# Performance work log

Measured on AMD Instinct MI355X. Metric: run time of the kernel, lower is better.

## Reference

```python
import jax, jax.numpy as jnp
import numpy as np

N = 100000          # total nodes
F = 128             # in_features
B = 1000            # number of graphs
NPG = 100           # nodes per graph (contiguous)
DEG = 16            # avg degree
E = B * NPG * DEG   # total edges (intra-graph)
K_RATIO = 0.8
KNUM = max(1, int(K_RATIO * NPG))  # nodes kept per graph = 80


def setup_inputs() -> dict:
    key = jax.random.key(0)
    k1, k2, k3, k4 = jax.random.split(key, 4)
    x = jax.random.normal(k1, (N, F), dtype=jnp.float32)
    # intra-graph random edges: offset each block of NPG*DEG edges by its graph's base node id
    offs = (jnp.arange(E, dtype=jnp.int32) // (NPG * DEG)) * NPG
    src = jax.random.randint(k2, (E,), 0, NPG, dtype=jnp.int32) + offs
    dst = jax.random.randint(k3, (E,), 0, NPG, dtype=jnp.int32) + offs
    edge_index = jnp.stack([src, dst], axis=0)
    batch = (jnp.arange(N, dtype=jnp.int32) // NPG).astype(jnp.int32)
    limit = float(np.sqrt(6.0 / (F + 1)))  # xavier_uniform for (F,1)
    theta_att = jax.random.uniform(k4, (F, 1), dtype=jnp.float32, minval=-limit, maxval=limit)
    return {"x": x, "edge_index": edge_index, "batch": batch, "theta_att": theta_att}


def reference(x, edge_index, batch, theta_att):
    num_nodes = x.shape[0]
    # add self loops with weight 1
    loops = jnp.arange(num_nodes, dtype=edge_index.dtype)
    row = jnp.concatenate([edge_index[0], loops])
    col = jnp.concatenate([edge_index[1], loops])
    w = jnp.ones(row.shape[0], dtype=x.dtype)
    # symmetric degree normalization (degree counted over row, as in torch code)
    deg = jax.ops.segment_sum(w, row, num_segments=num_nodes)
    dis = jnp.where(deg > 0, jax.lax.rsqrt(deg), jnp.zeros((), x.dtype))
    norm = dis[row] * w * dis[col]
    # scatter-add: agg[dst] += x[src] * norm
    agg = jax.ops.segment_sum(x[row] * norm[:, None], col, num_segments=num_nodes)
    z = (agg @ theta_att)[:, 0]                     # (N,)
    # per-graph top-k: graphs are contiguous and equal-sized -> reshape
    zb = z.reshape(B, NPG)
    _, pos = jax.lax.top_k(zb, KNUM)                # (B, KNUM) positions within each graph
    pos = jnp.sort(pos, axis=1)                     # global sort of keep_idx == per-graph sort here
    keep = (pos + jnp.arange(B, dtype=pos.dtype)[:, None] * NPG).reshape(-1)  # (B*KNUM,)
    scale = jax.nn.sigmoid(z[keep])[:, None]
    x_new = x[keep] * scale                         # (B*KNUM, F)
    batch_new = batch[keep]
    # subgraph with relabeled nodes; dropped edges padded with -1 (fixed shape for jit)
    node_mask = jnp.zeros(num_nodes, dtype=bool).at[keep].set(True)
    new_id = jnp.cumsum(node_mask.astype(jnp.int32)) - 1
    emask = node_mask[edge_index[0]] & node_mask[edge_index[1]]
    edge_index_new = jnp.where(emask[None, :], new_id[edge_index], -1)
    return x_new, edge_index_new, batch_new
```

## Files before the change

kernel.cpp:

```cpp
#include <hip/hip_runtime.h>


#define NPG   100
#define EPG   1600
#define KNUM  80
#define FDIM  128
#define NF4   (NPG * FDIM / 4)
#define NE4   (EPG / 4)

__global__ __launch_bounds__(256)
void sagpool_fused3(const float* __restrict__ x,
                    const int*   __restrict__ ei,
                    const float* __restrict__ theta,
                    float* __restrict__ out,
                    int E_total, int out_x_elems)
{
    const int g    = blockIdx.x;
    const int tid  = threadIdx.x;
    const int wave = tid >> 6;
    const int lane = tid & 63;
    const int base = g * NPG;

    __shared__ int4   sh_edge4[NE4];
    __shared__ int    sh_deg[NPG];
    __shared__ double sh_s[NPG];
    __shared__ double sh_dis[NPG];
    __shared__ double sh_a[NPG];
    __shared__ double sh_zp[4][NPG];
    __shared__ double sh_z[NPG];
    __shared__ unsigned long long sh_mask[2];
    __shared__ int    sh_newid[NPG];
    __shared__ int    sh_keepnode[KNUM];
    __shared__ float  sh_scale[KNUM];

    int* sh_edge = (int*)sh_edge4;

    const float4 th = ((const float4*)theta)[lane & 31];

    if (tid < NPG) sh_deg[tid] = 1;
    for (int i = tid; i < 4 * NPG; i += 256) ((double*)sh_zp)[i] = 0.0;
    __syncthreads();

    const int4* src4 = (const int4*)(ei + (size_t)g * EPG);
    const int4* dst4 = (const int4*)(ei + (size_t)E_total + (size_t)g * EPG);
    const bool  hasE1 = tid < (NE4 - 256);
    int4 es0 = src4[tid];
    int4 ed0 = dst4[tid];
    int4 es1, ed1;
    if (hasE1) { es1 = src4[256 + tid]; ed1 = dst4[256 + tid]; }

    const float4* xb4 = (const float4*)(x + (size_t)base * FDIM);
    float4 v[12];
    #pragma unroll
    for (int i = 0; i < 12; ++i) v[i] = xb4[i * 256 + tid];
    const bool has13 = tid < (NF4 - 12 * 256);
    float4 v12;
    if (has13) v12 = xb4[12 * 256 + tid];

    {
        int4 s4 = es0, d4 = ed0;
        s4.x -= base; s4.y -= base; s4.z -= base; s4.w -= base;
        d4.x -= base; d4.y -= base; d4.z -= base; d4.w -= base;
        int4 p; p.x = s4.x | (d4.x << 16); p.y = s4.y | (d4.y << 16);
                p.z = s4.z | (d4.z << 16); p.w = s4.w | (d4.w << 16);
        sh_edge4[tid] = p;
        atomicAdd(&sh_deg[s4.x], 1); atomicAdd(&sh_deg[s4.y], 1);
        atomicAdd(&sh_deg[s4.z], 1); atomicAdd(&sh_deg[s4.w], 1);
    }
    if (hasE1) {
        int4 s4 = es1, d4 = ed1;
        s4.x -= base; s4.y -= base; s4.z -= base; s4.w -= base;
        d4.x -= base; d4.y -= base; d4.z -= base; d4.w -= base;
        int4 p; p.x = s4.x | (d4.x << 16); p.y = s4.y | (d4.y << 16);
                p.z = s4.z | (d4.z << 16); p.w = s4.w | (d4.w << 16);
        sh_edge4[256 + tid] = p;
        atomicAdd(&sh_deg[s4.x], 1); atomicAdd(&sh_deg[s4.y], 1);
        atomicAdd(&sh_deg[s4.z], 1); atomicAdd(&sh_deg[s4.w], 1);
    }

    #pragma unroll
    for (int i = 0; i < 12; ++i) {
        double p = (double)v[i].x * th.x + (double)v[i].y * th.y
                 + (double)v[i].z * th.z + (double)v[i].w * th.w;
        #pragma unroll
        for (int m = 1; m <= 16; m <<= 1) p += __shfl_xor(p, m, 64);
        if ((lane & 31) == 0) sh_s[(i * 256 + tid) >> 5] = p;
    }
    if (tid < 128) {
        double p = (double)v12.x * th.x + (double)v12.y * th.y
                 + (double)v12.z * th.z + (double)v12.w * th.w;
        #pragma unroll
        for (int m = 1; m <= 16; m <<= 1) p += __shfl_xor(p, m, 64);
        if ((lane & 31) == 0) sh_s[(12 * 256 + tid) >> 5] = p;
    }
    __syncthreads();

    if (tid < NPG) {
        double dis = 1.0 / sqrt((double)sh_deg[tid]);
        sh_dis[tid] = dis;
        sh_a[tid]   = sh_s[tid] * dis;
    }
    __syncthreads();

    {
        double* zp = sh_zp[wave];
        for (int j = tid; j < EPG; j += 256) {
            int p = sh_edge[j];
            int s = p & 0xffff;
            int d = p >> 16;
            atomicAdd(&zp[d], sh_a[s] * sh_dis[d]);
        }
    }
    __syncthreads();

    double zi = 0.0;
    if (tid < NPG) {
        zi = sh_a[tid] * sh_dis[tid]
           + sh_zp[0][tid] + sh_zp[1][tid] + sh_zp[2][tid] + sh_zp[3][tid];
        sh_z[tid] = zi;
    }
    __syncthreads();

    bool kept = false;
    if (tid < NPG) {
        int rank = 0;
        for (int j = 0; j < NPG; ++j) {
            double zj = sh_z[j];
            rank += (int)((zj > zi) | ((zj == zi) & (j < tid)));
        }
        kept = rank < KNUM;
        sh_newid[tid] = -1;
    }
    unsigned long long m = __ballot(kept);
    if (lane == 0 && wave < 2) sh_mask[wave] = m;
    __syncthreads();

    if (kept) {
        int before = (wave == 0)
            ? __popcll(sh_mask[0] & ((1ull << lane) - 1ull))
            : __popcll(sh_mask[0]) + __popcll(sh_mask[1] & ((1ull << lane) - 1ull));
        int row = g * KNUM + before;
        sh_newid[tid]       = row;
        sh_keepnode[before] = tid;
        sh_scale[before]    = (float)(1.0 / (1.0 + exp(-zi)));
        out[(size_t)out_x_elems + 2 * (size_t)E_total + row] = (float)g;
    }
    __syncthreads();

    for (int idx = tid; idx < KNUM * FDIM / 4; idx += 256) {
        int   row  = idx >> 5;
        int   c    = idx & 31;
        int   node = sh_keepnode[row];
        float sc   = sh_scale[row];
        float4 xv  = ((const float4*)(x + (size_t)(base + node) * FDIM))[c];
        float4 o;
        o.x = xv.x * sc; o.y = xv.y * sc; o.z = xv.z * sc; o.w = xv.w * sc;
        ((float4*)(out + (size_t)(g * KNUM + row) * FDIM))[c] = o;
    }

    float* e0 = out + out_x_elems;
    float* e1 = e0 + E_total;
    for (int slot = tid; slot < NE4; slot += 256) {
        int4 p = sh_edge4[slot];
        float4 o0, o1;
        {
            int s = p.x & 0xffff, d = p.x >> 16;
            int a = sh_newid[s], b = sh_newid[d];
            bool vv = (a >= 0) && (b >= 0);
            o0.x = vv ? (float)a : -1.0f; o1.x = vv ? (float)b : -1.0f;
        }
        {
            int s = p.y & 0xffff, d = p.y >> 16;
            int a = sh_newid[s], b = sh_newid[d];
            bool vv = (a >= 0) && (b >= 0);
            o0.y = vv ? (float)a : -1.0f; o1.y = vv ? (float)b : -1.0f;
        }
        {
            int s = p.z & 0xffff, d = p.z >> 16;
            int a = sh_newid[s], b = sh_newid[d];
            bool vv = (a >= 0) && (b >= 0);
            o0.z = vv ? (float)a : -1.0f; o1.z = vv ? (float)b : -1.0f;
        }
        {
            int s = p.w & 0xffff, d = p.w >> 16;
            int a = sh_newid[s], b = sh_newid[d];
            bool vv = (a >= 0) && (b >= 0);
            o0.w = vv ? (float)a : -1.0f; o1.w = vv ? (float)b : -1.0f;
        }
        ((float4*)e0)[(size_t)g * NE4 + slot] = o0;
        ((float4*)e1)[(size_t)g * NE4 + slot] = o1;
    }
}

extern "C" void kernel_launch(void* const* d_in, const int* in_sizes, int n_in,
                              void* d_out, int out_size, void* d_ws, size_t ws_size,
                              hipStream_t stream)
{
    const float* x     = (const float*)d_in[0];
    const int*   ei    = (const int*)d_in[1];
    const float* theta = (const float*)d_in[3];
    float* out = (float*)d_out;

    const int N = in_sizes[0] / FDIM;
    const int E = in_sizes[1] / 2;
    const int B = N / NPG;
    const int out_x_elems = B * KNUM * FDIM;

    sagpool_fused3<<<dim3(B), dim3(256), 0, stream>>>(x, ei, theta, out, E, out_x_elems);
}
```

Measured before the change: 115.7 us.

## Reuse register-held x rows for output and widen block to 512 threads

The output write of kept rows now reuses the x values already held in registers from the attention dot product, instead of re-reading kept rows from global memory. This removes the second global read of x. Each thread writes its row only if that node was kept, scaled by a per-node sigmoid stored in shared memory. The block also grows from 256 to 512 threads, with eight per-wave partial accumulators, so each thread holds fewer float4s and there are more waves per block, at the cost of register and occupancy trade-offs.

```diff
diff --git a/kernel.cpp b/kernel.cpp
--- a/kernel.cpp
+++ b/kernel.cpp
@@ -5,11 +5,13 @@
 #define EPG   1600
 #define KNUM  80
 #define FDIM  128
+#define BT    512
 #define NF4   (NPG * FDIM / 4)
 #define NE4   (EPG / 4)
-
-__global__ __launch_bounds__(256)
-void sagpool_fused3(const float* __restrict__ x,
+#define NCH   (NF4 / BT)
+
+__global__ __launch_bounds__(BT)
+void sagpool_fused4(const float* __restrict__ x,
                     const int*   __restrict__ ei,
                     const float* __restrict__ theta,
                     float* __restrict__ out,
@@ -26,39 +28,35 @@
     __shared__ double sh_s[NPG];
     __shared__ double sh_dis[NPG];
     __shared__ double sh_a[NPG];
-    __shared__ double sh_zp[4][NPG];
+    __shared__ double sh_zp[8][NPG];
     __shared__ double sh_z[NPG];
     __shared__ unsigned long long sh_mask[2];
     __shared__ int    sh_newid[NPG];
-    __shared__ int    sh_keepnode[KNUM];
-    __shared__ float  sh_scale[KNUM];
-
+    __shared__ float  sh_scalen[NPG];
     int* sh_edge = (int*)sh_edge4;
 
     const float4 th = ((const float4*)theta)[lane & 31];
 
     if (tid < NPG) sh_deg[tid] = 1;
-    for (int i = tid; i < 4 * NPG; i += 256) ((double*)sh_zp)[i] = 0.0;
+    for (int i = tid; i < 8 * NPG; i += BT) ((double*)sh_zp)[i] = 0.0;
     __syncthreads();
 
     const int4* src4 = (const int4*)(ei + (size_t)g * EPG);
     const int4* dst4 = (const int4*)(ei + (size_t)E_total + (size_t)g * EPG);
-    const bool  hasE1 = tid < (NE4 - 256);
-    int4 es0 = src4[tid];
-    int4 ed0 = dst4[tid];
-    int4 es1, ed1;
-    if (hasE1) { es1 = src4[256 + tid]; ed1 = dst4[256 + tid]; }
+    const bool  hasE = tid < NE4;
+    int4 es, ed;
+    if (hasE) { es = src4[tid]; ed = dst4[tid]; }
 
     const float4* xb4 = (const float4*)(x + (size_t)base * FDIM);
-    float4 v[12];
+    float4 v[NCH];
     #pragma unroll
-    for (int i = 0; i < 12; ++i) v[i] = xb4[i * 256 + tid];
-    const bool has13 = tid < (NF4 - 12 * 256);
-    float4 v12;
-    if (has13) v12 = xb4[12 * 256 + tid];
-
-    {
-        int4 s4 = es0, d4 = ed0;
+    for (int i = 0; i < NCH; ++i) v[i] = xb4[i * BT + tid];
+    const bool hasR = tid < (NF4 - NCH * BT);
+    float4 vR;
+    if (hasR) vR = xb4[NCH * BT + tid];
+
+    if (hasE) {
+        int4 s4 = es, d4 = ed;
         s4.x -= base; s4.y -= base; s4.z -= base; s4.w -= base;
         d4.x -= base; d4.y -= base; d4.z -= base; d4.w -= base;
         int4 p; p.x = s4.x | (d4.x << 16); p.y = s4.y | (d4.y << 16);
@@ -67,31 +65,21 @@
         atomicAdd(&sh_deg[s4.x], 1); atomicAdd(&sh_deg[s4.y], 1);
         atomicAdd(&sh_deg[s4.z], 1); atomicAdd(&sh_deg[s4.w], 1);
     }
-    if (hasE1) {
-        int4 s4 = es1, d4 = ed1;
-        s4.x -= base; s4.y -= base; s4.z -= base; s4.w -= base;
-        d4.x -= base; d4.y -= base; d4.z -= base; d4.w -= base;
-        int4 p; p.x = s4.x | (d4.x << 16); p.y = s4.y | (d4.y << 16);
-                p.z = s4.z | (d4.z << 16); p.w = s4.w | (d4.w << 16);
-        sh_edge4[256 + tid] = p;
-        atomicAdd(&sh_deg[s4.x], 1); atomicAdd(&sh_deg[s4.y], 1);
-        atomicAdd(&sh_deg[s4.z], 1); atomicAdd(&sh_deg[s4.w], 1);
-    }
 
     #pragma unroll
-    for (int i = 0; i < 12; ++i) {
+    for (int i = 0; i < NCH; ++i) {
         double p = (double)v[i].x * th.x + (double)v[i].y * th.y
                  + (double)v[i].z * th.z + (double)v[i].w * th.w;
         #pragma unroll
         for (int m = 1; m <= 16; m <<= 1) p += __shfl_xor(p, m, 64);
-        if ((lane & 31) == 0) sh_s[(i * 256 + tid) >> 5] = p;
-    }
-    if (tid < 128) {
-        double p = (double)v12.x * th.x + (double)v12.y * th.y
-                 + (double)v12.z * th.z + (double)v12.w * th.w;
+        if ((lane & 31) == 0) sh_s[(i * BT + tid) >> 5] = p;
+    }
+    if (hasR) {
+        double p = (double)vR.x * th.x + (double)vR.y * th.y
+                 + (double)vR.z * th.z + (double)vR.w * th.w;
         #pragma unroll
         for (int m = 1; m <= 16; m <<= 1) p += __shfl_xor(p, m, 64);
-        if ((lane & 31) == 0) sh_s[(12 * 256 + tid) >> 5] = p;
+        if ((lane & 31) == 0) sh_s[(NCH * BT + tid) >> 5] = p;
     }
     __syncthreads();
 
@@ -104,7 +92,7 @@
 
     {
         double* zp = sh_zp[wave];
-        for (int j = tid; j < EPG; j += 256) {
+        for (int j = tid; j < EPG; j += BT) {
             int p = sh_edge[j];
             int s = p & 0xffff;
             int d = p >> 16;
@@ -116,7 +104,8 @@
     double zi = 0.0;
     if (tid < NPG) {
         zi = sh_a[tid] * sh_dis[tid]
-           + sh_zp[0][tid] + sh_zp[1][tid] + sh_zp[2][tid] + sh_zp[3][tid];
+           + sh_zp[0][tid] + sh_zp[1][tid] + sh_zp[2][tid] + sh_zp[3][tid]
+           + sh_zp[4][tid] + sh_zp[5][tid] + sh_zp[6][tid] + sh_zp[7][tid];
         sh_z[tid] = zi;
     }
     __syncthreads();
@@ -140,28 +129,43 @@
             ? __popcll(sh_mask[0] & ((1ull << lane) - 1ull))
             : __popcll(sh_mask[0]) + __popcll(sh_mask[1] & ((1ull << lane) - 1ull));
         int row = g * KNUM + before;
-        sh_newid[tid]       = row;
-        sh_keepnode[before] = tid;
-        sh_scale[before]    = (float)(1.0 / (1.0 + exp(-zi)));
+        sh_newid[tid]   = row;
+        sh_scalen[tid]  = (float)(1.0 / (1.0 + exp(-zi)));
         out[(size_t)out_x_elems + 2 * (size_t)E_total + row] = (float)g;
     }
     __syncthreads();
 
-    for (int idx = tid; idx < KNUM * FDIM / 4; idx += 256) {
-        int   row  = idx >> 5;
-        int   c    = idx & 31;
-        int   node = sh_keepnode[row];
-        float sc   = sh_scale[row];
-        float4 xv  = ((const float4*)(x + (size_t)(base + node) * FDIM))[c];
-        float4 o;
-        o.x = xv.x * sc; o.y = xv.y * sc; o.z = xv.z * sc; o.w = xv.w * sc;
-        ((float4*)(out + (size_t)(g * KNUM + row) * FDIM))[c] = o;
+    float4* outx = (float4*)out;
+    #pragma unroll
+    for (int i = 0; i < NCH; ++i) {
+        int idx = i * BT + tid;
+        int row = idx >> 5;
+        int nid = sh_newid[row];
+        if (nid >= 0) {
+            float sc = sh_scalen[row];
+            float4 o;
+            o.x = v[i].x * sc; o.y = v[i].y * sc;
+            o.z = v[i].z * sc; o.w = v[i].w * sc;
+            outx[(size_t)nid * 32 + (idx & 31)] = o;
+        }
+    }
+    if (hasR) {
+        int idx = NCH * BT + tid;
+        int row = idx >> 5;
+        int nid = sh_newid[row];
+        if (nid >= 0) {
+            float sc = sh_scalen[row];
+            float4 o;
+            o.x = vR.x * sc; o.y = vR.y * sc;
+            o.z = vR.z * sc; o.w = vR.w * sc;
+            outx[(size_t)nid * 32 + (idx & 31)] = o;
+        }
     }
 
     float* e0 = out + out_x_elems;
     float* e1 = e0 + E_total;
-    for (int slot = tid; slot < NE4; slot += 256) {
-        int4 p = sh_edge4[slot];
+    if (hasE) {
+        int4 p = sh_edge4[tid];
         float4 o0, o1;
         {
             int s = p.x & 0xffff, d = p.x >> 16;
@@ -187,8 +191,8 @@
             bool vv = (a >= 0) && (b >= 0);
             o0.w = vv ? (float)a : -1.0f; o1.w = vv ? (float)b : -1.0f;
         }
-        ((float4*)e0)[(size_t)g * NE4 + slot] = o0;
-        ((float4*)e1)[(size_t)g * NE4 + slot] = o1;
+        ((float4*)e0)[(size_t)g * NE4 + tid] = o0;
+        ((float4*)e1)[(size_t)g * NE4 + tid] = o1;
     }
 }
 
@@ -206,5 +210,5 @@
     const int B = N / NPG;
     const int out_x_elems = B * KNUM * FDIM;
 
-    sagpool_fused3<<<dim3(B), dim3(256), 0, stream>>>(x, ei, theta, out, E, out_x_elems);
+    sagpool_fused4<<<dim3(B), dim3(BT), 0, stream>>>(x, ei, theta, out, E, out_x_elems);
 }
```

Measured after the change: 110.6 us. -4.4%, faster.
